# Kernel optimization log

Hardware: AMD Instinct MI355X
Metric: run time of the kernel (lower is better)

Reference implementation:

```python
import jax, jax.numpy as jnp
import numpy as np

D_MODEL = 1024
H = 16
D_K = D_MODEL // H


def setup_inputs() -> dict:
    key = jax.random.key(0)
    ks = jax.random.split(key, 12)
    B, S = 4, 2048
    s = 1.0 / np.sqrt(D_MODEL)
    return {
        "Q": jax.random.normal(ks[0], (B, S, D_MODEL), jnp.float32),
        "K": jax.random.normal(ks[1], (B, S, D_MODEL), jnp.float32),
        "V": jax.random.normal(ks[2], (B, S, D_MODEL), jnp.float32),
        "attn_mask": jnp.ones((B, S), jnp.int32),
        "Wq": jax.random.normal(ks[3], (D_MODEL, D_MODEL), jnp.float32) * s,
        "bq": jax.random.normal(ks[4], (D_MODEL,), jnp.float32) * s,
        "Wk": jax.random.normal(ks[5], (D_MODEL, D_MODEL), jnp.float32) * s,
        "bk": jax.random.normal(ks[6], (D_MODEL,), jnp.float32) * s,
        "Wv": jax.random.normal(ks[7], (D_MODEL, D_MODEL), jnp.float32) * s,
        "bv": jax.random.normal(ks[8], (D_MODEL,), jnp.float32) * s,
        "Wo": jax.random.normal(ks[9], (D_MODEL, D_MODEL), jnp.float32) * s,
        "bo": jax.random.normal(ks[10], (D_MODEL,), jnp.float32) * s,
    }


def _split_heads(x):
    B, S, _ = x.shape
    return x.reshape(B, S, H, D_K).transpose(0, 2, 1, 3)  # (B,H,S,Dk)


def reference(Q, K, V, attn_mask, Wq, bq, Wk, bk, Wv, bv, Wo, bo):
    # Linear projections (torch Linear: x @ W.T + b)
    q = _split_heads(Q @ Wq.T + bq)
    k = _split_heads(K @ Wk.T + bk)
    v = _split_heads(V @ Wv.T + bv)
    scale = 1.0 / jnp.sqrt(jnp.asarray(D_K, q.dtype))
    scores = jnp.einsum("bhqd,bhkd->bhqk", q, k) * scale  # (B,H,S,S)
    # 2-D mask (B,S) broadcast over heads and query positions; 0 -> -inf
    mask = attn_mask[:, None, None, :]
    scores = jnp.where(mask == 0, -jnp.inf, scores)
    attn = jax.nn.softmax(scores, axis=-1)
    # dropout_proba = 0.0 -> identity
    x = jnp.einsum("bhqk,bhkd->bhqd", attn, v)
    B, _, S, _ = x.shape
    x = x.transpose(0, 2, 1, 3).reshape(B, S, D_MODEL)
    return x @ Wo.T + bo
```

## Files before the change

### kernel.cpp

```cpp
#include <hip/hip_runtime.h>
#include <stdint.h>

typedef unsigned short u16;
typedef __attribute__((ext_vector_type(8))) unsigned short u16x8;
typedef __attribute__((ext_vector_type(4))) unsigned short u16x4;
typedef __attribute__((ext_vector_type(2))) __fp16 h16x2;
typedef __attribute__((ext_vector_type(4))) _Float16 f16x4;
typedef __attribute__((ext_vector_type(8))) _Float16 f16x8;
typedef __attribute__((ext_vector_type(4))) float f32x4;

#define MFMA16F16(a,b,c)  __builtin_amdgcn_mfma_f32_16x16x16f16((a),(b),(c),0,0,0)
#define MFMA32F16(a,b,c)  __builtin_amdgcn_mfma_f32_16x16x32_f16((a),(b),(c),0,0,0)

__device__ __forceinline__ f32x4 f4zero() {
    f32x4 z; z[0]=0.f; z[1]=0.f; z[2]=0.f; z[3]=0.f; return z;
}
__device__ __forceinline__ u16x8 cvth8(float4 a, float4 b) {
    union { h16x2 h[4]; u16x8 u; } U;
    U.h[0] = __builtin_amdgcn_cvt_pkrtz(a.x, a.y);
    U.h[1] = __builtin_amdgcn_cvt_pkrtz(a.z, a.w);
    U.h[2] = __builtin_amdgcn_cvt_pkrtz(b.x, b.y);
    U.h[3] = __builtin_amdgcn_cvt_pkrtz(b.z, b.w);
    return U.u;
}

#define GLDS(gp, lp) __builtin_amdgcn_global_load_lds( \
    (const __attribute__((address_space(1))) void*)(gp), \
    (__attribute__((address_space(3))) void*)(lp), 16, 0, 0)

#define QSC 0.1803368801111601f

__global__ __launch_bounds__(256) void conv_w(
    const float* __restrict__ w0, const float* __restrict__ w1,
    const float* __restrict__ w2, const float* __restrict__ w3,
    u16* __restrict__ out)
{
    const int t = blockIdx.x >> 8;
    const float* src = (t == 0) ? w0 : (t == 1) ? w1 : (t == 2) ? w2 : w3;
    const size_t idx = (size_t)(blockIdx.x & 255) * 4096 + (size_t)threadIdx.x * 16;
    u16* dst = out + (size_t)t * 1048576 + idx;
    float4 a0 = *(const float4*)(src + idx);
    float4 a1 = *(const float4*)(src + idx + 4);
    float4 a2 = *(const float4*)(src + idx + 8);
    float4 a3 = *(const float4*)(src + idx + 12);
    *(u16x8*)dst       = cvth8(a0, a1);
    *(u16x8*)(dst + 8) = cvth8(a2, a3);
}

__global__ __launch_bounds__(256) void conv_x(
    const float* __restrict__ x0, const float* __restrict__ x1,
    const float* __restrict__ x2, u16* __restrict__ out)
{
    const int t = blockIdx.y;
    const float* src = (t == 0) ? x0 : (t == 1) ? x1 : x2;
    const size_t idx = (size_t)blockIdx.x * 4096 + (size_t)threadIdx.x * 16;
    u16* dst = out + (size_t)t * 8388608 + idx;
    float4 a0 = *(const float4*)(src + idx);
    float4 a1 = *(const float4*)(src + idx + 4);
    float4 a2 = *(const float4*)(src + idx + 8);
    float4 a3 = *(const float4*)(src + idx + 12);
    *(u16x8*)dst       = cvth8(a0, a1);
    *(u16x8*)(dst + 8) = cvth8(a2, a3);
}

template<int MODE>
__global__ __launch_bounds__(256, 3) void gemm_qkv(
    const float* __restrict__ Qf, const float* __restrict__ Kf, const float* __restrict__ Vf,
    const u16* __restrict__ xc, const u16* __restrict__ wc,
    const float* __restrict__ Wqf, const float* __restrict__ Wkf, const float* __restrict__ Wvf,
    const float* __restrict__ bq, const float* __restrict__ bk, const float* __restrict__ bv,
    u16* __restrict__ qhp, u16* __restrict__ khp, u16* __restrict__ vtp)
{
    __shared__ __align__(16) char smem[34816];
    u16* As = (u16*)smem;
    u16* Bs = As + 4096;
    u16* Ct = (u16*)smem;

    const int t  = blockIdx.y >> 3;
    const int n0 = (blockIdx.y & 7) * 128;
    const int m0 = blockIdx.x * 128;
    const float* X    = (t == 0) ? Qf : (t == 1) ? Kf : Vf;
    const float* Wf   = (t == 0) ? Wqf : (t == 1) ? Wkf : Wvf;
    const float* bias = (t == 0) ? bq : (t == 1) ? bk : bv;
    const u16*   Wb   = wc + (size_t)t * 1048576;
    const u16*   Xc   = xc + (size_t)t * 8388608;
    u16*         dst  = (t == 0) ? qhp : (t == 1) ? khp : vtp;
    const float  scl  = (t == 0) ? QSC : 1.0f;

    const int tid  = threadIdx.x;
    const int wave = tid >> 6, lane = tid & 63;
    const int quad = lane >> 4, l16 = lane & 15;
    const int wm = (wave >> 1) * 64, wn = (wave & 1) * 64;

    const int c0 = wave, c1 = wave + 4;
    const size_t gl = (size_t)(lane >> 2) * 1024 + (lane & 3) * 8;
    const int sr = tid >> 1, hh = tid & 1;
    const size_t xrow = (size_t)(m0 + sr) * 1024 + hh * 16;
    const size_t wrow = (size_t)(n0 + sr) * 1024 + hh * 16;

    f32x4 acc[4][4];
    for (int i = 0; i < 4; i++) for (int j = 0; j < 4; j++) acc[i][j] = f4zero();

    for (int k0 = 0; k0 < 1024; k0 += 32) {
        if (MODE == 2) {
            GLDS(Xc + (size_t)(m0 + c0 * 16) * 1024 + gl + k0, As + c0 * 512);
            GLDS(Xc + (size_t)(m0 + c1 * 16) * 1024 + gl + k0, As + c1 * 512);
        } else {
            float4 a0 = *(const float4*)(X + xrow + k0);
            float4 a1 = *(const float4*)(X + xrow + k0 + 4);
            float4 a2 = *(const float4*)(X + xrow + k0 + 8);
            float4 a3 = *(const float4*)(X + xrow + k0 + 12);
            *(u16x8*)(As + sr * 32 + hh * 16)     = cvth8(a0, a1);
            *(u16x8*)(As + sr * 32 + hh * 16 + 8) = cvth8(a2, a3);
        }
        if (MODE >= 1) {
            GLDS(Wb + (size_t)(n0 + c0 * 16) * 1024 + gl + k0, Bs + c0 * 512);
            GLDS(Wb + (size_t)(n0 + c1 * 16) * 1024 + gl + k0, Bs + c1 * 512);
        } else {
            float4 b0 = *(const float4*)(Wf + wrow + k0);
            float4 b1 = *(const float4*)(Wf + wrow + k0 + 4);
            float4 b2 = *(const float4*)(Wf + wrow + k0 + 8);
            float4 b3 = *(const float4*)(Wf + wrow + k0 + 12);
            *(u16x8*)(Bs + sr * 32 + hh * 16)     = cvth8(b0, b1);
            *(u16x8*)(Bs + sr * 32 + hh * 16 + 8) = cvth8(b2, b3);
        }
        __syncthreads();

        f16x8 af[4], bfr[4];
#pragma unroll
        for (int i = 0; i < 4; i++) {
            af[i]  = *(const f16x8*)(As + (wm + i * 16 + l16) * 32 + quad * 8);
            bfr[i] = *(const f16x8*)(Bs + (wn + i * 16 + l16) * 32 + quad * 8);
        }
#pragma unroll
        for (int i = 0; i < 4; i++)
#pragma unroll
            for (int j = 0; j < 4; j++)
                acc[i][j] = MFMA32F16(af[i], bfr[j], acc[i][j]);
        __syncthreads();
    }

#pragma unroll
    for (int i = 0; i < 4; i++) {
        const int row = wm + i * 16 + quad * 4;
#pragma unroll
        for (int j = 0; j < 4; j++) {
            const int col = wn + j * 16 + l16;
            const float bv2 = bias[n0 + col];
#pragma unroll
            for (int r = 0; r < 2; r++) {
                union { h16x2 h; unsigned u; } P;
                P.h = __builtin_amdgcn_cvt_pkrtz((acc[i][j][2*r] + bv2) * scl,
                                                 (acc[i][j][2*r+1] + bv2) * scl);
                Ct[(row + 2*r)     * 136 + col] = (u16)(P.u & 0xFFFF);
                Ct[(row + 2*r + 1) * 136 + col] = (u16)(P.u >> 16);
            }
        }
    }
    __syncthreads();

    if (t < 2) {
        const int row = tid >> 1, half = tid & 1;
        const int m = m0 + row, b = m >> 11, s = m & 2047;
        const int h = (n0 >> 6) + half;
        u16* o = dst + ((size_t)(b * 16 + h) * 2048 + s) * 64;
        const u16* src = Ct + row * 136 + half * 64;
#pragma unroll
        for (int j = 0; j < 64; j += 8) *(u16x8*)(o + j) = *(const u16x8*)(src + j);
    } else {
        const int col = tid >> 1, shalf = tid & 1;
        const int h = (n0 >> 6) + (col >> 6), d = col & 63;
        const int mb = m0 + shalf * 64, b = mb >> 11, sb = mb & 2047;
        u16* o = dst + (size_t)((b * 16 + h) * 64 + d) * 2048 + sb;
#pragma unroll
        for (int j0 = 0; j0 < 64; j0 += 8) {
            u16x8 tv;
#pragma unroll
            for (int j = 0; j < 8; j++) tv[j] = Ct[(shalf * 64 + j0 + j) * 136 + col];
            *(u16x8*)(o + j0) = tv;
        }
    }
}

template<bool WGLDS>
__global__ __launch_bounds__(256, 3) void gemm_o(
    const u16* __restrict__ Xb, const u16* __restrict__ wcO,
    const float* __restrict__ Wf, const float* __restrict__ bias,
    float* __restrict__ out)
{
    __shared__ __align__(16) u16 As[4096];
    __shared__ __align__(16) u16 Bs[4096];

    const int tid  = threadIdx.x;
    const int wave = tid >> 6, lane = tid & 63;
    const int quad = lane >> 4, l16 = lane & 15;
    const int m0 = blockIdx.x * 128, n0 = blockIdx.y * 128;
    const int wm = (wave >> 1) * 64, wn = (wave & 1) * 64;

    const int c0 = wave, c1 = wave + 4;
    const size_t gl = (size_t)(lane >> 2) * 1024 + (lane & 3) * 8;
    const int sr = tid >> 1, hh = tid & 1;
    const size_t wrow = (size_t)(n0 + sr) * 1024 + hh * 16;

    f32x4 acc[4][4];
    for (int i = 0; i < 4; i++) for (int j = 0; j < 4; j++) acc[i][j] = f4zero();

    for (int k0 = 0; k0 < 1024; k0 += 32) {
        GLDS(Xb + (size_t)(m0 + c0 * 16) * 1024 + gl + k0, As + c0 * 512);
        GLDS(Xb + (size_t)(m0 + c1 * 16) * 1024 + gl + k0, As + c1 * 512);
        if (WGLDS) {
            GLDS(wcO + (size_t)(n0 + c0 * 16) * 1024 + gl + k0, Bs + c0 * 512);
            GLDS(wcO + (size_t)(n0 + c1 * 16) * 1024 + gl + k0, Bs + c1 * 512);
        } else {
            float4 b0 = *(const float4*)(Wf + wrow + k0);
            float4 b1 = *(const float4*)(Wf + wrow + k0 + 4);
            float4 b2 = *(const float4*)(Wf + wrow + k0 + 8);
            float4 b3 = *(const float4*)(Wf + wrow + k0 + 12);
            *(u16x8*)(Bs + sr * 32 + hh * 16)     = cvth8(b0, b1);
            *(u16x8*)(Bs + sr * 32 + hh * 16 + 8) = cvth8(b2, b3);
        }
        __syncthreads();

        f16x8 af[4], bfr[4];
#pragma unroll
        for (int i = 0; i < 4; i++) {
            af[i]  = *(const f16x8*)(As + (wm + i * 16 + l16) * 32 + quad * 8);
            bfr[i] = *(const f16x8*)(Bs + (wn + i * 16 + l16) * 32 + quad * 8);
        }
#pragma unroll
        for (int i = 0; i < 4; i++)
#pragma unroll
            for (int j = 0; j < 4; j++)
                acc[i][j] = MFMA32F16(af[i], bfr[j], acc[i][j]);
        __syncthreads();
    }

#pragma unroll
    for (int i = 0; i < 4; i++)
#pragma unroll
        for (int j = 0; j < 4; j++) {
            const int col = wn + j * 16 + l16;
            const float bv = bias[n0 + col];
#pragma unroll
            for (int r = 0; r < 4; r++)
                out[(size_t)(m0 + wm + i * 16 + quad * 4 + r) * 1024 + n0 + col] = acc[i][j][r] + bv;
        }
}

__global__ __launch_bounds__(256, 4) void attn_fused(
    const u16* __restrict__ qh, const u16* __restrict__ kh,
    const u16* __restrict__ vth, const int* __restrict__ mask,
    u16* __restrict__ xout)
{
    __shared__ __align__(16) u16 Ksh[2][4096];
    __shared__ __align__(16) u16 Vsh[2][4352];
    __shared__ float mshf[2][64];

    const int tid = threadIdx.x, wave = tid >> 6, lane = tid & 63;
    const int quad = lane >> 4, l16 = lane & 15;

    const int flat = blockIdx.x + (blockIdx.y << 4);
    const int xr = flat & 7, xc_ = flat >> 3;
    const int qb = xc_ & 15, bh = xr + ((xc_ >> 4) << 3);
    const int b = bh >> 4, h = bh & 15;
    const int wq = qb * 128 + wave * 32;

    f16x8 qf[2][2];
#pragma unroll
    for (int qg = 0; qg < 2; qg++)
#pragma unroll
        for (int kc = 0; kc < 2; kc++)
            qf[qg][kc] = *(const f16x8*)(qh + ((size_t)bh * 2048 + wq + qg * 16 + l16) * 64
                                         + kc * 32 + quad * 8);

    f32x4 o[2][4];
#pragma unroll
    for (int qg = 0; qg < 2; qg++)
        for (int dt = 0; dt < 4; dt++) o[qg][dt] = f4zero();
    f32x4 lacc[2]; lacc[0] = f4zero(); lacc[1] = f4zero();
    f16x4 ones;
    ones[0] = (_Float16)1.f; ones[1] = (_Float16)1.f;
    ones[2] = (_Float16)1.f; ones[3] = (_Float16)1.f;

    const int klr = lane >> 3;
    const size_t kgoff = (size_t)((lane & 7) ^ klr) << 3;
    const u16* kgb = kh + (size_t)bh * 2048 * 64;

    const int skey = tid >> 2, sc = (tid & 3) * 16;
    const u16* vg = vth + ((size_t)bh * 64 + skey) * 2048 + sc;
    const int mrow = b * 2048;

    {
        GLDS(kgb + (size_t)(wave * 16 + klr) * 64 + kgoff,     &Ksh[0][wave * 1024]);
        GLDS(kgb + (size_t)(wave * 16 + 8 + klr) * 64 + kgoff, &Ksh[0][wave * 1024 + 512]);
        const u16x8 v0 = *(const u16x8*)(vg);
        const u16x8 v1 = *(const u16x8*)(vg + 8);
        u16* vd = &Vsh[0][skey * 68 + sc];
        *(u16x4*)(vd)      = (u16x4){v0[0], v0[1], v0[2], v0[3]};
        *(u16x4*)(vd + 4)  = (u16x4){v0[4], v0[5], v0[6], v0[7]};
        *(u16x4*)(vd + 8)  = (u16x4){v1[0], v1[1], v1[2], v1[3]};
        *(u16x4*)(vd + 12) = (u16x4){v1[4], v1[5], v1[6], v1[7]};
        if (tid < 64) mshf[0][tid] = mask[mrow + tid] ? -10.0f : -1.0e30f;
    }
    __syncthreads();

    for (int t = 0; t < 32; ++t) {
        const int cur = t & 1;
        const u16* Kc = &Ksh[cur][0];
        const u16* Vc = &Vsh[cur][0];

        u16x8 v0, v1; int mreg = 1;
        const int kk2 = (t + 1) * 64;
        if (t < 31) {
            GLDS(kgb + (size_t)(kk2 + wave * 16 + klr) * 64 + kgoff,
                 &Ksh[cur ^ 1][wave * 1024]);
            GLDS(kgb + (size_t)(kk2 + wave * 16 + 8 + klr) * 64 + kgoff,
                 &Ksh[cur ^ 1][wave * 1024 + 512]);
            v0 = *(const u16x8*)(vg + kk2);
            v1 = *(const u16x8*)(vg + kk2 + 8);
            if (tid < 64) mreg = mask[mrow + kk2 + tid];
        }

        __builtin_amdgcn_s_setprio(1);
#pragma unroll
        for (int nt = 0; nt < 4; nt++) {
            const int kro = (nt * 16 + l16) * 64;
            const f16x8 kf0 = *(const f16x8*)(Kc + kro + ((quad ^ (l16 & 7)) << 3));
            const f16x8 kf1 = *(const f16x8*)(Kc + kro + (((quad ^ 4) ^ (l16 & 7)) << 3));
            const float4 mb = *(const float4*)(&mshf[cur][nt * 16 + quad * 4]);
            f16x4 pf[2];
#pragma unroll
            for (int qg = 0; qg < 2; qg++) {
                f32x4 z;
                z[0] = mb.x; z[1] = mb.y; z[2] = mb.z; z[3] = mb.w;
                z = MFMA32F16(kf0, qf[qg][0], z);
                z = MFMA32F16(kf1, qf[qg][1], z);
                union { h16x2 h[2]; f16x4 v; } U;
                U.h[0] = __builtin_amdgcn_cvt_pkrtz(__builtin_amdgcn_exp2f(z[0]),
                                                    __builtin_amdgcn_exp2f(z[1]));
                U.h[1] = __builtin_amdgcn_cvt_pkrtz(__builtin_amdgcn_exp2f(z[2]),
                                                    __builtin_amdgcn_exp2f(z[3]));
                pf[qg] = U.v;
            }
            lacc[0] = MFMA16F16(ones, pf[0], lacc[0]);
            lacc[1] = MFMA16F16(ones, pf[1], lacc[1]);
#pragma unroll
            for (int dt = 0; dt < 4; dt++) {
                const f16x4 vf = *(const f16x4*)(Vc + (dt * 16 + l16) * 68 + nt * 16 + quad * 4);
                o[0][dt] = MFMA16F16(vf, pf[0], o[0][dt]);
                o[1][dt] = MFMA16F16(vf, pf[1], o[1][dt]);
            }
        }
        __builtin_amdgcn_s_setprio(0);

        if (t < 31) {
            u16* vd = &Vsh[cur ^ 1][skey * 68 + sc];
            *(u16x4*)(vd)      = (u16x4){v0[0], v0[1], v0[2], v0[3]};
            *(u16x4*)(vd + 4)  = (u16x4){v0[4], v0[5], v0[6], v0[7]};
            *(u16x4*)(vd + 8)  = (u16x4){v1[0], v1[1], v1[2], v1[3]};
            *(u16x4*)(vd + 12) = (u16x4){v1[4], v1[5], v1[6], v1[7]};
            if (tid < 64) mshf[cur ^ 1][tid] = mreg ? -10.0f : -1.0e30f;
        }
        __syncthreads();
    }

#pragma unroll
    for (int qg = 0; qg < 2; qg++) {
        const float inv = 1.0f / lacc[qg][0];
        const int row = wq + qg * 16 + l16;
        u16* op = xout + ((size_t)b * 2048 + row) * 1024 + h * 64;
#pragma unroll
        for (int dt = 0; dt < 4; dt++) {
            union { h16x2 h[2]; u16x4 u; } U;
            U.h[0] = __builtin_amdgcn_cvt_pkrtz(o[qg][dt][0] * inv, o[qg][dt][1] * inv);
            U.h[1] = __builtin_amdgcn_cvt_pkrtz(o[qg][dt][2] * inv, o[qg][dt][3] * inv);
            *(u16x4*)(op + dt * 16 + quad * 4) = U.u;
        }
    }
}

extern "C" void kernel_launch(void* const* d_in, const int* in_sizes, int n_in,
                              void* d_out, int out_size, void* d_ws, size_t ws_size,
                              hipStream_t stream)
{
    const float* Q   = (const float*)d_in[0];
    const float* K   = (const float*)d_in[1];
    const float* V   = (const float*)d_in[2];
    const int*   msk = (const int*)d_in[3];
    const float* Wq  = (const float*)d_in[4];
    const float* bq  = (const float*)d_in[5];
    const float* Wk  = (const float*)d_in[6];
    const float* bk  = (const float*)d_in[7];
    const float* Wv  = (const float*)d_in[8];
    const float* bv  = (const float*)d_in[9];
    const float* Wo  = (const float*)d_in[10];
    const float* bo  = (const float*)d_in[11];

    u16* base = (u16*)d_ws;
    dim3 blk(256);
    dim3 gq(64, 24);
    dim3 ga(16, 64);
    dim3 go(64, 8);

    if (ws_size >= 109051904UL) {
        u16* wc  = base;
        u16* xc  = base + 4194304;
        u16* qhp = xc + 25165824;
        u16* khp = qhp + 8388608;
        u16* vtp = khp + 8388608;
        u16* xs  = xc;
        conv_w<<<1024, blk, 0, stream>>>(Wq, Wk, Wv, Wo, wc);
        conv_x<<<dim3(2048, 3), blk, 0, stream>>>(Q, K, V, xc);
        gemm_qkv<2><<<gq, blk, 0, stream>>>(Q, K, V, xc, wc,
            nullptr, nullptr, nullptr, bq, bk, bv, qhp, khp, vtp);
        attn_fused<<<ga, blk, 0, stream>>>(qhp, khp, vtp, msk, xs);
        gemm_o<true><<<go, blk, 0, stream>>>(xs, wc + 3 * 1048576, nullptr, bo, (float*)d_out);
    } else if (ws_size >= ((size_t)72 << 20)) {
        u16* wc  = base;
        u16* qhp = base + 4194304;
        u16* khp = qhp + 8388608;
        u16* vtp = khp + 8388608;
        u16* xs  = vtp + 8388608;
        conv_w<<<1024, blk, 0, stream>>>(Wq, Wk, Wv, Wo, wc);
        gemm_qkv<1><<<gq, blk, 0, stream>>>(Q, K, V, nullptr, wc,
            nullptr, nullptr, nullptr, bq, bk, bv, qhp, khp, vtp);
        attn_fused<<<ga, blk, 0, stream>>>(qhp, khp, vtp, msk, xs);
        gemm_o<true><<<go, blk, 0, stream>>>(xs, wc + 3 * 1048576, nullptr, bo, (float*)d_out);
    } else {
        u16* qhp = base;
        u16* khp = qhp + 8388608;
        u16* vtp = khp + 8388608;
        u16* xs  = vtp + 8388608;
        gemm_qkv<0><<<gq, blk, 0, stream>>>(Q, K, V, nullptr, nullptr,
            Wq, Wk, Wv, bq, bk, bv, qhp, khp, vtp);
        attn_fused<<<ga, blk, 0, stream>>>(qhp, khp, vtp, msk, xs);
        gemm_o<false><<<go, blk, 0, stream>>>(xs, nullptr, Wo, bo, (float*)d_out);
    }
}
```

Measured before the change: 354.4 us.

## Deepen GEMM K-tile to 64 with XOR-swizzled LDS and merge conversion kernels

Both projection GEMMs now stage 64-wide K slices per iteration instead of 32, using an XOR-swizzled LDS row layout. The swizzle is applied to both the global_load_lds writes and the fragment reads. This halves the number of barrier pairs per GEMM and is meant to avoid LDS bank conflicts on the 128-byte row stride. The weight and activation fp16 conversion kernels are merged into a single launch to cut one kernel launch. LDS use per block doubles to 32KB, which may limit occupancy.

```diff
diff --git a/kernel.cpp b/kernel.cpp
--- a/kernel.cpp
+++ b/kernel.cpp
@@ -29,6 +29,37 @@
     (__attribute__((address_space(3))) void*)(lp), 16, 0, 0)
 
 #define QSC 0.1803368801111601f
+
+__global__ __launch_bounds__(256) void conv_all(
+    const float* __restrict__ w0, const float* __restrict__ w1,
+    const float* __restrict__ w2, const float* __restrict__ w3,
+    const float* __restrict__ x0, const float* __restrict__ x1,
+    const float* __restrict__ x2,
+    u16* __restrict__ wout, u16* __restrict__ xout)
+{
+    int bx = blockIdx.x;
+    const float* src; u16* dst;
+    if (bx < 1024) {
+        const int t = bx >> 8;
+        src = (t == 0) ? w0 : (t == 1) ? w1 : (t == 2) ? w2 : w3;
+        const size_t idx = (size_t)(bx & 255) * 4096 + (size_t)threadIdx.x * 16;
+        src += idx;
+        dst = wout + (size_t)t * 1048576 + idx;
+    } else {
+        bx -= 1024;
+        const int t = bx >> 11;
+        src = (t == 0) ? x0 : (t == 1) ? x1 : x2;
+        const size_t idx = (size_t)(bx & 2047) * 4096 + (size_t)threadIdx.x * 16;
+        src += idx;
+        dst = xout + (size_t)t * 8388608 + idx;
+    }
+    float4 a0 = *(const float4*)(src);
+    float4 a1 = *(const float4*)(src + 4);
+    float4 a2 = *(const float4*)(src + 8);
+    float4 a3 = *(const float4*)(src + 12);
+    *(u16x8*)dst       = cvth8(a0, a1);
+    *(u16x8*)(dst + 8) = cvth8(a2, a3);
+}
 
 __global__ __launch_bounds__(256) void conv_w(
     const float* __restrict__ w0, const float* __restrict__ w1,
@@ -47,22 +78,6 @@
     *(u16x8*)(dst + 8) = cvth8(a2, a3);
 }
 
-__global__ __launch_bounds__(256) void conv_x(
-    const float* __restrict__ x0, const float* __restrict__ x1,
-    const float* __restrict__ x2, u16* __restrict__ out)
-{
-    const int t = blockIdx.y;
-    const float* src = (t == 0) ? x0 : (t == 1) ? x1 : x2;
-    const size_t idx = (size_t)blockIdx.x * 4096 + (size_t)threadIdx.x * 16;
-    u16* dst = out + (size_t)t * 8388608 + idx;
-    float4 a0 = *(const float4*)(src + idx);
-    float4 a1 = *(const float4*)(src + idx + 4);
-    float4 a2 = *(const float4*)(src + idx + 8);
-    float4 a3 = *(const float4*)(src + idx + 12);
-    *(u16x8*)dst       = cvth8(a0, a1);
-    *(u16x8*)(dst + 8) = cvth8(a2, a3);
-}
-
 template<int MODE>
 __global__ __launch_bounds__(256, 3) void gemm_qkv(
     const float* __restrict__ Qf, const float* __restrict__ Kf, const float* __restrict__ Vf,
@@ -73,7 +88,7 @@
 {
     __shared__ __align__(16) char smem[34816];
     u16* As = (u16*)smem;
-    u16* Bs = As + 4096;
+    u16* Bs = As + 8192;
     u16* Ct = (u16*)smem;
 
     const int t  = blockIdx.y >> 3;
@@ -92,51 +107,63 @@
     const int quad = lane >> 4, l16 = lane & 15;
     const int wm = (wave >> 1) * 64, wn = (wave & 1) * 64;
 
-    const int c0 = wave, c1 = wave + 4;
-    const size_t gl = (size_t)(lane >> 2) * 1024 + (lane & 3) * 8;
+    const int grow = lane >> 3;
+    const size_t gsw = (size_t)(((lane & 7) ^ grow) << 3);
     const int sr = tid >> 1, hh = tid & 1;
-    const size_t xrow = (size_t)(m0 + sr) * 1024 + hh * 16;
-    const size_t wrow = (size_t)(n0 + sr) * 1024 + hh * 16;
+    const size_t xrow = (size_t)(m0 + sr) * 1024;
+    const size_t wrow = (size_t)(n0 + sr) * 1024;
 
     f32x4 acc[4][4];
     for (int i = 0; i < 4; i++) for (int j = 0; j < 4; j++) acc[i][j] = f4zero();
 
-    for (int k0 = 0; k0 < 1024; k0 += 32) {
+    for (int k0 = 0; k0 < 1024; k0 += 64) {
         if (MODE == 2) {
-            GLDS(Xc + (size_t)(m0 + c0 * 16) * 1024 + gl + k0, As + c0 * 512);
-            GLDS(Xc + (size_t)(m0 + c1 * 16) * 1024 + gl + k0, As + c1 * 512);
+#pragma unroll
+            for (int r = 0; r < 4; r++) {
+                const int row = wave * 32 + r * 8 + grow;
+                GLDS(Xc + (size_t)(m0 + row) * 1024 + k0 + gsw, As + wave * 2048 + r * 512);
+            }
         } else {
-            float4 a0 = *(const float4*)(X + xrow + k0);
-            float4 a1 = *(const float4*)(X + xrow + k0 + 4);
-            float4 a2 = *(const float4*)(X + xrow + k0 + 8);
-            float4 a3 = *(const float4*)(X + xrow + k0 + 12);
-            *(u16x8*)(As + sr * 32 + hh * 16)     = cvth8(a0, a1);
-            *(u16x8*)(As + sr * 32 + hh * 16 + 8) = cvth8(a2, a3);
+#pragma unroll
+            for (int c = 0; c < 4; c++) {
+                const int ch = hh * 4 + c;
+                float4 a0 = *(const float4*)(X + xrow + k0 + ch * 8);
+                float4 a1 = *(const float4*)(X + xrow + k0 + ch * 8 + 4);
+                *(u16x8*)(As + sr * 64 + ((ch ^ (sr & 7)) << 3)) = cvth8(a0, a1);
+            }
         }
         if (MODE >= 1) {
-            GLDS(Wb + (size_t)(n0 + c0 * 16) * 1024 + gl + k0, Bs + c0 * 512);
-            GLDS(Wb + (size_t)(n0 + c1 * 16) * 1024 + gl + k0, Bs + c1 * 512);
+#pragma unroll
+            for (int r = 0; r < 4; r++) {
+                const int row = wave * 32 + r * 8 + grow;
+                GLDS(Wb + (size_t)(n0 + row) * 1024 + k0 + gsw, Bs + wave * 2048 + r * 512);
+            }
         } else {
-            float4 b0 = *(const float4*)(Wf + wrow + k0);
-            float4 b1 = *(const float4*)(Wf + wrow + k0 + 4);
-            float4 b2 = *(const float4*)(Wf + wrow + k0 + 8);
-            float4 b3 = *(const float4*)(Wf + wrow + k0 + 12);
-            *(u16x8*)(Bs + sr * 32 + hh * 16)     = cvth8(b0, b1);
-            *(u16x8*)(Bs + sr * 32 + hh * 16 + 8) = cvth8(b2, b3);
+#pragma unroll
+            for (int c = 0; c < 4; c++) {
+                const int ch = hh * 4 + c;
+                float4 b0 = *(const float4*)(Wf + wrow + k0 + ch * 8);
+                float4 b1 = *(const float4*)(Wf + wrow + k0 + ch * 8 + 4);
+                *(u16x8*)(Bs + sr * 64 + ((ch ^ (sr & 7)) << 3)) = cvth8(b0, b1);
+            }
         }
         __syncthreads();
 
-        f16x8 af[4], bfr[4];
-#pragma unroll
-        for (int i = 0; i < 4; i++) {
-            af[i]  = *(const f16x8*)(As + (wm + i * 16 + l16) * 32 + quad * 8);
-            bfr[i] = *(const f16x8*)(Bs + (wn + i * 16 + l16) * 32 + quad * 8);
-        }
-#pragma unroll
-        for (int i = 0; i < 4; i++)
-#pragma unroll
-            for (int j = 0; j < 4; j++)
-                acc[i][j] = MFMA32F16(af[i], bfr[j], acc[i][j]);
+#pragma unroll
+        for (int kk = 0; kk < 2; kk++) {
+            f16x8 af[4], bfr[4];
+#pragma unroll
+            for (int i = 0; i < 4; i++) {
+                const int ra = wm + i * 16 + l16, rb = wn + i * 16 + l16;
+                af[i]  = *(const f16x8*)(As + ra * 64 + (((kk * 4 + quad) ^ (ra & 7)) << 3));
+                bfr[i] = *(const f16x8*)(Bs + rb * 64 + (((kk * 4 + quad) ^ (rb & 7)) << 3));
+            }
+#pragma unroll
+            for (int i = 0; i < 4; i++)
+#pragma unroll
+                for (int j = 0; j < 4; j++)
+                    acc[i][j] = MFMA32F16(af[i], bfr[j], acc[i][j]);
+        }
         __syncthreads();
     }
 
@@ -188,8 +215,8 @@
     const float* __restrict__ Wf, const float* __restrict__ bias,
     float* __restrict__ out)
 {
-    __shared__ __align__(16) u16 As[4096];
-    __shared__ __align__(16) u16 Bs[4096];
+    __shared__ __align__(16) u16 As[8192];
+    __shared__ __align__(16) u16 Bs[8192];
 
     const int tid  = threadIdx.x;
     const int wave = tid >> 6, lane = tid & 63;
@@ -197,41 +224,52 @@
     const int m0 = blockIdx.x * 128, n0 = blockIdx.y * 128;
     const int wm = (wave >> 1) * 64, wn = (wave & 1) * 64;
 
-    const int c0 = wave, c1 = wave + 4;
-    const size_t gl = (size_t)(lane >> 2) * 1024 + (lane & 3) * 8;
+    const int grow = lane >> 3;
+    const size_t gsw = (size_t)(((lane & 7) ^ grow) << 3);
     const int sr = tid >> 1, hh = tid & 1;
-    const size_t wrow = (size_t)(n0 + sr) * 1024 + hh * 16;
+    const size_t wrow = (size_t)(n0 + sr) * 1024;
 
     f32x4 acc[4][4];
     for (int i = 0; i < 4; i++) for (int j = 0; j < 4; j++) acc[i][j] = f4zero();
 
-    for (int k0 = 0; k0 < 1024; k0 += 32) {
-        GLDS(Xb + (size_t)(m0 + c0 * 16) * 1024 + gl + k0, As + c0 * 512);
-        GLDS(Xb + (size_t)(m0 + c1 * 16) * 1024 + gl + k0, As + c1 * 512);
+    for (int k0 = 0; k0 < 1024; k0 += 64) {
+#pragma unroll
+        for (int r = 0; r < 4; r++) {
+            const int row = wave * 32 + r * 8 + grow;
+            GLDS(Xb + (size_t)(m0 + row) * 1024 + k0 + gsw, As + wave * 2048 + r * 512);
+        }
         if (WGLDS) {
-            GLDS(wcO + (size_t)(n0 + c0 * 16) * 1024 + gl + k0, Bs + c0 * 512);
-            GLDS(wcO + (size_t)(n0 + c1 * 16) * 1024 + gl + k0, Bs + c1 * 512);
+#pragma unroll
+            for (int r = 0; r < 4; r++) {
+                const int row = wave * 32 + r * 8 + grow;
+                GLDS(wcO + (size_t)(n0 + row) * 1024 + k0 + gsw, Bs + wave * 2048 + r * 512);
+            }
         } else {
-            float4 b0 = *(const float4*)(Wf + wrow + k0);
-            float4 b1 = *(const float4*)(Wf + wrow + k0 + 4);
-            float4 b2 = *(const float4*)(Wf + wrow + k0 + 8);
-            float4 b3 = *(const float4*)(Wf + wrow + k0 + 12);
-            *(u16x8*)(Bs + sr * 32 + hh * 16)     = cvth8(b0, b1);
-            *(u16x8*)(Bs + sr * 32 + hh * 16 + 8) = cvth8(b2, b3);
+#pragma unroll
+            for (int c = 0; c < 4; c++) {
+                const int ch = hh * 4 + c;
+                float4 b0 = *(const float4*)(Wf + wrow + k0 + ch * 8);
+                float4 b1 = *(const float4*)(Wf + wrow + k0 + ch * 8 + 4);
+                *(u16x8*)(Bs + sr * 64 + ((ch ^ (sr & 7)) << 3)) = cvth8(b0, b1);
+            }
         }
         __syncthreads();
 
-        f16x8 af[4], bfr[4];
-#pragma unroll
-        for (int i = 0; i < 4; i++) {
-            af[i]  = *(const f16x8*)(As + (wm + i * 16 + l16) * 32 + quad * 8);
-            bfr[i] = *(const f16x8*)(Bs + (wn + i * 16 + l16) * 32 + quad * 8);
-        }
-#pragma unroll
-        for (int i = 0; i < 4; i++)
-#pragma unroll
-            for (int j = 0; j < 4; j++)
-                acc[i][j] = MFMA32F16(af[i], bfr[j], acc[i][j]);
+#pragma unroll
+        for (int kk = 0; kk < 2; kk++) {
+            f16x8 af[4], bfr[4];
+#pragma unroll
+            for (int i = 0; i < 4; i++) {
+                const int ra = wm + i * 16 + l16, rb = wn + i * 16 + l16;
+                af[i]  = *(const f16x8*)(As + ra * 64 + (((kk * 4 + quad) ^ (ra & 7)) << 3));
+                bfr[i] = *(const f16x8*)(Bs + rb * 64 + (((kk * 4 + quad) ^ (rb & 7)) << 3));
+            }
+#pragma unroll
+            for (int i = 0; i < 4; i++)
+#pragma unroll
+                for (int j = 0; j < 4; j++)
+                    acc[i][j] = MFMA32F16(af[i], bfr[j], acc[i][j]);
+        }
         __syncthreads();
     }
 
@@ -409,8 +447,7 @@
         u16* khp = qhp + 8388608;
         u16* vtp = khp + 8388608;
         u16* xs  = xc;
-        conv_w<<<1024, blk, 0, stream>>>(Wq, Wk, Wv, Wo, wc);
-        conv_x<<<dim3(2048, 3), blk, 0, stream>>>(Q, K, V, xc);
+        conv_all<<<7168, blk, 0, stream>>>(Wq, Wk, Wv, Wo, Q, K, V, wc, xc);
         gemm_qkv<2><<<gq, blk, 0, stream>>>(Q, K, V, xc, wc,
             nullptr, nullptr, nullptr, bq, bk, bv, qhp, khp, vtp);
         attn_fused<<<ga, blk, 0, stream>>>(qhp, khp, vtp, msk, xs);
```

Result: no change. 357.4 us (+0.8%).
